# Kernel tuning notes

Hardware: AMD Instinct MI355X
Metric: run time of the kernel (lower is better)

## Reference

```python
import jax, jax.numpy as jnp
import numpy as np

GRID_NUM = 5   # number of grid intervals (pykan default)
SPLINE_K = 3   # B-spline degree (pykan default)
GRID_RANGE = (-1.0, 1.0)


def make_grid(in_dim):
    # Extended uniform grid: num + 2k + 1 knots per input dim, shared values.
    h = (GRID_RANGE[1] - GRID_RANGE[0]) / GRID_NUM
    pts = GRID_RANGE[0] + h * jnp.arange(-SPLINE_K, GRID_NUM + SPLINE_K + 1, dtype=jnp.float32)
    return jnp.broadcast_to(pts, (in_dim, pts.shape[0]))  # (in_dim, num+2k+1)


def bspline_basis(x, grid, k):
    # Cox-de Boor recursion. x: (n, d); grid: (d, m). Returns (n, d, m-1-k).
    xe = x[..., None]            # (n, d, 1)
    g = grid[None]               # (1, d, m)
    B = ((xe >= g[..., :-1]) & (xe < g[..., 1:])).astype(x.dtype)
    for p in range(1, k + 1):
        left = (xe - g[..., :-(p + 1)]) / (g[..., p:-1] - g[..., :-(p + 1)])
        right = (g[..., p + 1:] - xe) / (g[..., p + 1:] - g[..., 1:-p])
        B = left * B[..., :-1] + right * B[..., 1:]
    return B


def kan_layer(x, coef, scale_base, scale_sp, grid):
    # x: (n, in); coef: (in, out, G+k); scales: (in, out)
    basis = bspline_basis(x, grid, SPLINE_K)              # (n, in, G+k)
    base = jax.nn.silu(x)                                 # (n, in)
    # y[n,o] = sum_i scale_base[i,o]*silu(x[n,i]) + scale_sp[i,o]*sum_g B[n,i,g]*coef[i,o,g]
    spline = jnp.einsum('nig,iog->no', basis, coef * scale_sp[:, :, None])
    return base @ scale_base + spline


def setup_inputs() -> dict:
    key = jax.random.key(0)
    ks = jax.random.split(key, 5)
    b, s, hid, ffn = 2, 4096, 512, 2048
    nb = GRID_NUM + SPLINE_K  # 8 basis functions
    x = jax.random.normal(ks[0], (b, s, hid), dtype=jnp.float32)
    coef1 = 0.1 * jax.random.normal(ks[1], (hid, ffn, nb), dtype=jnp.float32)
    scale_base1 = (1.0 / np.sqrt(hid)) * jax.random.normal(ks[2], (hid, ffn), dtype=jnp.float32)
    scale_sp1 = jnp.ones((hid, ffn), dtype=jnp.float32)
    coef2 = 0.1 * jax.random.normal(ks[3], (ffn, hid, nb), dtype=jnp.float32)
    scale_base2 = (1.0 / np.sqrt(ffn)) * jax.random.normal(ks[4], (ffn, hid), dtype=jnp.float32)
    scale_sp2 = jnp.ones((ffn, hid), dtype=jnp.float32)
    return {'x': x, 'coef1': coef1, 'scale_base1': scale_base1, 'scale_sp1': scale_sp1,
            'coef2': coef2, 'scale_base2': scale_base2, 'scale_sp2': scale_sp2}


def reference(x, coef1, scale_base1, scale_sp1, coef2, scale_base2, scale_sp2):
    b, s, hid = x.shape
    ffn = coef1.shape[1]
    grid1 = make_grid(hid)   # non-trainable buffers, derived from defaults
    grid2 = make_grid(ffn)
    h = x.reshape(b * s, hid)                     # rearrange 'b s h -> (b s) h'
    h = kan_layer(h, coef1, scale_base1, scale_sp1, grid1)
    h = kan_layer(h, coef2, scale_base2, scale_sp2, grid2)
    return h.reshape(b, s, hid)
```

## Files before the change

kernel.cpp:

```cpp
#include <hip/hip_runtime.h>
#include <cstdint>
#include <cstddef>

typedef _Float16 f16;
typedef _Float16 f16x8 __attribute__((ext_vector_type(8)));
typedef float f32x4 __attribute__((ext_vector_type(4)));

__device__ __forceinline__ void async16(const void* g, void* l) {
  __builtin_amdgcn_global_load_lds(
      (const __attribute__((address_space(1))) unsigned int*)g,
      (__attribute__((address_space(3))) unsigned int*)l,
      16, 0, 0);
}

template <int I, int O>
__global__ void prep_coef(const float* __restrict__ coef,
                          const float* __restrict__ ssp,
                          f16* __restrict__ Wt) {
  int tid = blockIdx.x * 256 + threadIdx.x;
  if (tid >= I * O) return;
  int i = tid / O, o = tid % O;
  float s = ssp[tid];
  const float* c = coef + (size_t)tid * 8;
  f16x8 out;
#pragma unroll
  for (int g = 0; g < 8; ++g) out[g] = (f16)(c[g] * s);
  *(f16x8*)(Wt + (size_t)o * (I * 9) + (size_t)i * 8) = out;
}

template <int I, int O>
__global__ void prep_base(const float* __restrict__ sb, f16* __restrict__ Wt) {
  int tid = blockIdx.x * 256 + threadIdx.x;
  if (tid >= I * O) return;
  int o = tid / I, i = tid % I;
  Wt[(size_t)o * (I * 9) + (size_t)I * 8 + i] = (f16)sb[(size_t)i * O + o];
}

__device__ __forceinline__ f16x8 spline8(float h) {
  float v = __builtin_fmaf(2.5f, h, 5.5f);
  float c = floorf(v);
  float f = v - c;
  float f2 = f * f, f3 = f2 * f;
  float b3 = f3 * (1.f / 6.f);
  float t = 1.f - f;
  float b0 = t * t * t * (1.f / 6.f);
  float b1 = (2.f / 3.f) - f2 + 0.5f * f3;
  float b2 = 1.f - b0 - b1 - b3;
  unsigned int u01 =
      __builtin_bit_cast(unsigned int, __builtin_amdgcn_cvt_pkrtz(b0, b1));
  unsigned int u23 =
      __builtin_bit_cast(unsigned int, __builtin_amdgcn_cvt_pkrtz(b2, b3));
  unsigned long long pk = (unsigned long long)u01 |
                          ((unsigned long long)u23 << 32);
  int ci = (int)c;
  int s = (ci - 3) * 16;
  __uint128_t r = 0;
  if (s >= 0) {
    if (s < 128) r = (__uint128_t)pk << s;
  } else {
    int q = -s;
    if (q < 64) r = (__uint128_t)(pk >> q);
  }
  return __builtin_bit_cast(f16x8, r);
}

template <int I, int ATOMIC>
__global__ __launch_bounds__(256, 2) void gemm_kan(const float* __restrict__ H,
                                                   const f16* __restrict__ W,
                                                   float* __restrict__ C,
                                                   int N, int kChunk) {
  constexpr int K = 9 * I;
  constexpr int KB = 8 * I;
  __shared__ __align__(16) f16 sA[128 * 64];
  __shared__ __align__(16) f16 sB[256 * 64];
  const int t = threadIdx.x;
  const int n0 = blockIdx.x * 256;
  const int m0 = blockIdx.y * 128;
  const int kBeg = blockIdx.z * kChunk;
  const int kEnd = kBeg + kChunk;
  const int w = t >> 6, lane = t & 63;
  const int wm = (w >> 1) * 64, wn = (w & 1) * 128;
  const int lr = lane & 15, lq = lane >> 4;
  const int wbase = t & 192;
  const int srow = t >> 3;
  const int j_ = t & 7;
  const int js = j_ ^ (srow & 7);

  f32x4 acc[4][8] = {};
  const f16* Wrow = W + (size_t)(n0 + srow) * K + js * 8;
  const float* Hrow = H + (size_t)(m0 + srow) * I;

  float hs[4];
  if (kBeg < KB) {
    const int i0 = kBeg >> 3;
#pragma unroll
    for (int q = 0; q < 4; ++q)
      hs[q] = Hrow[(size_t)(q * 32) * I + i0 + j_];
  }

  for (int k0 = kBeg; k0 < kEnd; k0 += 64) {
#pragma unroll
    for (int q = 0; q < 8; ++q)
      async16(Wrow + (size_t)(q * 32) * K + k0, &sB[(q * 256 + wbase) * 8]);

    if (k0 < KB) {
#pragma unroll
      for (int q = 0; q < 4; ++q)
        *(f16x8*)&sA[((q * 32 + srow) * 8 + js) * 8] = spline8(hs[q]);
      const int kn = k0 + 64;
      if (kn < kEnd && kn < KB) {
        const int i0n = kn >> 3;
#pragma unroll
        for (int q = 0; q < 4; ++q)
          hs[q] = Hrow[(size_t)(q * 32) * I + i0n + j_];
      }
    } else {
      const int c0 = (k0 - KB) + j_ * 8;
      f32x4 ha[4][2];
#pragma unroll
      for (int q = 0; q < 4; ++q) {
        const f32x4* p = (const f32x4*)(Hrow + (size_t)(q * 32) * I + c0);
        ha[q][0] = p[0];
        ha[q][1] = p[1];
      }
#pragma unroll
      for (int q = 0; q < 4; ++q) {
        f16x8 o;
#pragma unroll
        for (int s = 0; s < 8; ++s) {
          float h = ha[q][s >> 2][s & 3];
          o[s] = (f16)(h / (1.f + __expf(-h)));
        }
        *(f16x8*)&sA[((q * 32 + srow) * 8 + js) * 8] = o;
      }
    }
    __syncthreads();
#pragma unroll
    for (int kk = 0; kk < 64; kk += 32) {
      f16x8 av[4], bv[8];
#pragma unroll
      for (int i = 0; i < 4; ++i) {
        const int ra = wm + i * 16 + lr;
        const int ca = ((kk >> 3) + lq) ^ (ra & 7);
        av[i] = *(const f16x8*)&sA[ra * 64 + ca * 8];
      }
#pragma unroll
      for (int j = 0; j < 8; ++j) {
        const int rb = wn + j * 16 + lr;
        const int cb = ((kk >> 3) + lq) ^ (rb & 7);
        bv[j] = *(const f16x8*)&sB[rb * 64 + cb * 8];
      }
#pragma unroll
      for (int i = 0; i < 4; ++i)
#pragma unroll
        for (int j = 0; j < 8; ++j)
          acc[i][j] = __builtin_amdgcn_mfma_f32_16x16x32_f16(av[i], bv[j],
                                                             acc[i][j], 0, 0, 0);
    }
    __syncthreads();
  }

#pragma unroll
  for (int i = 0; i < 4; ++i) {
#pragma unroll
    for (int j = 0; j < 8; ++j) {
      const int col = n0 + wn + j * 16 + lr;
#pragma unroll
      for (int r = 0; r < 4; ++r) {
        const int row = m0 + wm + i * 16 + lq * 4 + r;
        if (ATOMIC)
          atomicAdd(&C[(size_t)row * N + col], acc[i][j][r]);
        else
          C[(size_t)row * N + col] = acc[i][j][r];
      }
    }
  }
}

extern "C" void kernel_launch(void* const* d_in, const int* in_sizes, int n_in,
                              void* d_out, int out_size, void* d_ws,
                              size_t ws_size, hipStream_t stream) {
  const float* x     = (const float*)d_in[0];
  const float* coef1 = (const float*)d_in[1];
  const float* sb1   = (const float*)d_in[2];
  const float* ssp1  = (const float*)d_in[3];
  const float* coef2 = (const float*)d_in[4];
  const float* sb2   = (const float*)d_in[5];
  const float* ssp2  = (const float*)d_in[6];

  const int Mtot = 8192;
  const int I1 = 512, O1 = 2048, K1 = I1 * 9;
  const int I2 = 2048, O2 = 512, K2 = I2 * 9;

  char* ws = (char*)d_ws;
  const size_t szW1 = (size_t)O1 * K1 * sizeof(f16);
  const size_t szW2 = (size_t)O2 * K2 * sizeof(f16);
  const size_t szH  = (size_t)Mtot * O1 * sizeof(float);
  if (ws_size < szW1 + szW2 + szH) return;
  f16*   W1 = (f16*)ws;
  f16*   W2 = (f16*)(ws + szW1);
  float* h1 = (float*)(ws + szW1 + szW2);

  {
    int n1 = I1 * O1;
    prep_coef<512, 2048><<<(n1 + 255) / 256, 256, 0, stream>>>(coef1, ssp1, W1);
    prep_base<512, 2048><<<(n1 + 255) / 256, 256, 0, stream>>>(sb1, W1);
    int n2 = I2 * O2;
    prep_coef<2048, 512><<<(n2 + 255) / 256, 256, 0, stream>>>(coef2, ssp2, W2);
    prep_base<2048, 512><<<(n2 + 255) / 256, 256, 0, stream>>>(sb2, W2);
  }

  gemm_kan<512, 0><<<dim3(O1 / 256, Mtot / 128, 1), 256, 0, stream>>>(
      x, W1, h1, O1, K1);

  (void)hipMemsetAsync(d_out, 0, (size_t)Mtot * O2 * sizeof(float), stream);
  const int SK = 4;
  gemm_kan<2048, 1><<<dim3(O2 / 256, Mtot / 128, SK), 256, 0, stream>>>(
      h1, W2, (float*)d_out, O2, K2 / SK);
}
```

Baseline: 546.2 us.

## Pre-swizzle weights into MFMA fragment layout and load B directly to registers

The prep kernels now write the fp16 weight matrix in a tiled layout where each 16-column by 32-k block is stored contiguously in MFMA B-fragment order, so each lane can read its operand with one 16-byte global load. The GEMM drops the async global-to-LDS staging and the LDS buffer for B, loading B fragments straight into registers and prefetching the second k-half while the first half's MFMAs run. prep_base is also vectorised to emit 8 values per thread. This removes LDS traffic and LDS capacity for B, which may allow higher occupancy, but B is no longer shared across the two warps that cover the same columns, so global and L2 reads of W double and load latency sits directly on the MFMA path.

```diff
diff --git a/kernel.cpp b/kernel.cpp
--- a/kernel.cpp
+++ b/kernel.cpp
@@ -6,17 +6,12 @@
 typedef _Float16 f16x8 __attribute__((ext_vector_type(8)));
 typedef float f32x4 __attribute__((ext_vector_type(4)));
 
-__device__ __forceinline__ void async16(const void* g, void* l) {
-  __builtin_amdgcn_global_load_lds(
-      (const __attribute__((address_space(1))) unsigned int*)g,
-      (__attribute__((address_space(3))) unsigned int*)l,
-      16, 0, 0);
-}
 
 template <int I, int O>
 __global__ void prep_coef(const float* __restrict__ coef,
                           const float* __restrict__ ssp,
                           f16* __restrict__ Wt) {
+  constexpr int K32 = (9 * I) / 32;
   int tid = blockIdx.x * 256 + threadIdx.x;
   if (tid >= I * O) return;
   int i = tid / O, o = tid % O;
@@ -25,15 +20,24 @@
   f16x8 out;
 #pragma unroll
   for (int g = 0; g < 8; ++g) out[g] = (f16)(c[g] * s);
-  *(f16x8*)(Wt + (size_t)o * (I * 9) + (size_t)i * 8) = out;
+  size_t addr = ((size_t)(o >> 4) * K32 + (i >> 2)) * 512 +
+                (size_t)(((i & 3) * 16) + (o & 15)) * 8;
+  *(f16x8*)(Wt + addr) = out;
 }
 
 template <int I, int O>
 __global__ void prep_base(const float* __restrict__ sb, f16* __restrict__ Wt) {
+  constexpr int K32 = (9 * I) / 32;
   int tid = blockIdx.x * 256 + threadIdx.x;
-  if (tid >= I * O) return;
-  int o = tid / I, i = tid % I;
-  Wt[(size_t)o * (I * 9) + (size_t)I * 8 + i] = (f16)sb[(size_t)i * O + o];
+  if (tid >= (I / 8) * O) return;
+  int i8 = tid / O, o = tid % O;
+  f16x8 out;
+#pragma unroll
+  for (int s = 0; s < 8; ++s)
+    out[s] = (f16)sb[(size_t)(i8 * 8 + s) * O + o];
+  size_t addr = ((size_t)(o >> 4) * K32 + (I / 4) + (i8 >> 2)) * 512 +
+                (size_t)(((i8 & 3) * 16) + (o & 15)) * 8;
+  *(f16x8*)(Wt + addr) = out;
 }
 
 __device__ __forceinline__ f16x8 spline8(float h) {
@@ -71,8 +75,8 @@
                                                    int N, int kChunk) {
   constexpr int K = 9 * I;
   constexpr int KB = 8 * I;
+  constexpr int K32 = K / 32;
   __shared__ __align__(16) f16 sA[128 * 64];
-  __shared__ __align__(16) f16 sB[256 * 64];
   const int t = threadIdx.x;
   const int n0 = blockIdx.x * 256;
   const int m0 = blockIdx.y * 128;
@@ -81,14 +85,13 @@
   const int w = t >> 6, lane = t & 63;
   const int wm = (w >> 1) * 64, wn = (w & 1) * 128;
   const int lr = lane & 15, lq = lane >> 4;
-  const int wbase = t & 192;
   const int srow = t >> 3;
   const int j_ = t & 7;
   const int js = j_ ^ (srow & 7);
 
   f32x4 acc[4][8] = {};
-  const f16* Wrow = W + (size_t)(n0 + srow) * K + js * 8;
   const float* Hrow = H + (size_t)(m0 + srow) * I;
+  const f16* Pw = W + (size_t)((n0 + wn) >> 4) * K32 * 512 + lane * 8;
 
   float hs[4];
   if (kBeg < KB) {
@@ -99,9 +102,11 @@
   }
 
   for (int k0 = kBeg; k0 < kEnd; k0 += 64) {
-#pragma unroll
-    for (int q = 0; q < 8; ++q)
-      async16(Wrow + (size_t)(q * 32) * K + k0, &sB[(q * 256 + wbase) * 8]);
+    const int kb0 = k0 >> 5;
+    f16x8 bv0[8];
+#pragma unroll
+    for (int j = 0; j < 8; ++j)
+      bv0[j] = *(const f16x8*)(Pw + ((size_t)j * K32 + kb0) * 512);
 
     if (k0 < KB) {
 #pragma unroll
@@ -135,28 +140,35 @@
       }
     }
     __syncthreads();
-#pragma unroll
-    for (int kk = 0; kk < 64; kk += 32) {
-      f16x8 av[4], bv[8];
-#pragma unroll
-      for (int i = 0; i < 4; ++i) {
-        const int ra = wm + i * 16 + lr;
-        const int ca = ((kk >> 3) + lq) ^ (ra & 7);
-        av[i] = *(const f16x8*)&sA[ra * 64 + ca * 8];
-      }
-#pragma unroll
-      for (int j = 0; j < 8; ++j) {
-        const int rb = wn + j * 16 + lr;
-        const int cb = ((kk >> 3) + lq) ^ (rb & 7);
-        bv[j] = *(const f16x8*)&sB[rb * 64 + cb * 8];
-      }
-#pragma unroll
-      for (int i = 0; i < 4; ++i)
-#pragma unroll
-        for (int j = 0; j < 8; ++j)
-          acc[i][j] = __builtin_amdgcn_mfma_f32_16x16x32_f16(av[i], bv[j],
-                                                             acc[i][j], 0, 0, 0);
-    }
+
+    f16x8 av[4], bv1[8];
+#pragma unroll
+    for (int i = 0; i < 4; ++i) {
+      const int ra = wm + i * 16 + lr;
+      const int ca = lq ^ (ra & 7);
+      av[i] = *(const f16x8*)&sA[ra * 64 + ca * 8];
+    }
+#pragma unroll
+    for (int j = 0; j < 8; ++j)
+      bv1[j] = *(const f16x8*)(Pw + ((size_t)j * K32 + kb0 + 1) * 512);
+#pragma unroll
+    for (int i = 0; i < 4; ++i)
+#pragma unroll
+      for (int j = 0; j < 8; ++j)
+        acc[i][j] = __builtin_amdgcn_mfma_f32_16x16x32_f16(av[i], bv0[j],
+                                                           acc[i][j], 0, 0, 0);
+#pragma unroll
+    for (int i = 0; i < 4; ++i) {
+      const int ra = wm + i * 16 + lr;
+      const int ca = (4 + lq) ^ (ra & 7);
+      av[i] = *(const f16x8*)&sA[ra * 64 + ca * 8];
+    }
+#pragma unroll
+    for (int i = 0; i < 4; ++i)
+#pragma unroll
+      for (int j = 0; j < 8; ++j)
+        acc[i][j] = __builtin_amdgcn_mfma_f32_16x16x32_f16(av[i], bv1[j],
+                                                           acc[i][j], 0, 0, 0);
     __syncthreads();
   }
 
@@ -204,10 +216,10 @@
   {
     int n1 = I1 * O1;
     prep_coef<512, 2048><<<(n1 + 255) / 256, 256, 0, stream>>>(coef1, ssp1, W1);
-    prep_base<512, 2048><<<(n1 + 255) / 256, 256, 0, stream>>>(sb1, W1);
+    prep_base<512, 2048><<<(n1 / 8 + 255) / 256, 256, 0, stream>>>(sb1, W1);
     int n2 = I2 * O2;
     prep_coef<2048, 512><<<(n2 + 255) / 256, 256, 0, stream>>>(coef2, ssp2, W2);
-    prep_base<2048, 512><<<(n2 + 255) / 256, 256, 0, stream>>>(sb2, W2);
+    prep_base<2048, 512><<<(n2 / 8 + 255) / 256, 256, 0, stream>>>(sb2, W2);
   }
 
   gemm_kan<512, 0><<<dim3(O1 / 256, Mtot / 128, 1), 256, 0, stream>>>(
```

After: 522.1 us. 1.05x faster.
